# Kernel tuning notes

Hardware: AMD Instinct MI355X
Metric: run time of the kernel (lower is better)

Reference implementation:

```python
import jax, jax.numpy as jnp
import numpy as np

NUM_GRAPHS = 1024
IN_F = 256
HID = 512


def setup_inputs() -> dict:
    key = jax.random.key(0)
    ks = jax.random.split(key, 20)
    s_in = 1.0 / np.sqrt(IN_F)
    s_h = 1.0 / np.sqrt(HID)
    inp = {
        "x": jax.random.normal(ks[0], (200000, IN_F), dtype=jnp.float32),
        "batch": jnp.sort(jax.random.randint(ks[1], (200000,), 0, NUM_GRAPHS)),
        # transforms: Linear(in_features -> hidden)
        "W_mean": jax.random.uniform(ks[2], (IN_F, HID), jnp.float32, -s_in, s_in),
        "b_mean": jax.random.uniform(ks[3], (HID,), jnp.float32, -s_in, s_in),
        "W_max": jax.random.uniform(ks[4], (IN_F, HID), jnp.float32, -s_in, s_in),
        "b_max": jax.random.uniform(ks[5], (HID,), jnp.float32, -s_in, s_in),
        "W_sum": jax.random.uniform(ks[6], (IN_F, HID), jnp.float32, -s_in, s_in),
        "b_sum": jax.random.uniform(ks[7], (HID,), jnp.float32, -s_in, s_in),
        # gates: Linear(hidden -> 1) + sigmoid
        "g_mean_w": jax.random.uniform(ks[8], (HID, 1), jnp.float32, -s_h, s_h),
        "g_mean_b": jax.random.uniform(ks[9], (1,), jnp.float32, -s_h, s_h),
        "g_max_w": jax.random.uniform(ks[10], (HID, 1), jnp.float32, -s_h, s_h),
        "g_max_b": jax.random.uniform(ks[11], (1,), jnp.float32, -s_h, s_h),
        "g_sum_w": jax.random.uniform(ks[12], (HID, 1), jnp.float32, -s_h, s_h),
        "g_sum_b": jax.random.uniform(ks[13], (1,), jnp.float32, -s_h, s_h),
        # output proj: Linear(hidden -> in_features)
        "W_out": jax.random.uniform(ks[14], (HID, IN_F), jnp.float32, -s_h, s_h),
        "b_out": jax.random.uniform(ks[15], (IN_F,), jnp.float32, -s_h, s_h),
        # layer norm params
        "ln_gamma": jnp.ones((IN_F,), jnp.float32),
        "ln_beta": jnp.zeros((IN_F,), jnp.float32),
    }
    return inp


def reference(x, batch, W_mean, b_mean, W_max, b_max, W_sum, b_sum,
              g_mean_w, g_mean_b, g_max_w, g_max_b, g_sum_w, g_sum_b,
              W_out, b_out, ln_gamma, ln_beta):
    # --- segment pools over node dim ---
    sum_pool = jax.ops.segment_sum(x, batch, num_segments=NUM_GRAPHS)  # [G, F]
    counts = jax.ops.segment_sum(jnp.ones((x.shape[0],), x.dtype), batch,
                                 num_segments=NUM_GRAPHS)  # [G]
    mean_pool = sum_pool / jnp.maximum(counts, 1.0)[:, None]
    max_pool = jax.ops.segment_max(x, batch, num_segments=NUM_GRAPHS)
    max_pool = jnp.where(counts[:, None] > 0, max_pool, 0.0)

    # --- per-pool linear transforms ---
    mean_repr = mean_pool @ W_mean + b_mean  # [G, H]
    max_repr = max_pool @ W_max + b_max
    sum_repr = sum_pool @ W_sum + b_sum

    # --- gated fusion ---
    g_mean = jax.nn.sigmoid(mean_repr @ g_mean_w + g_mean_b)  # [G, 1]
    g_max = jax.nn.sigmoid(max_repr @ g_max_w + g_max_b)
    g_sum = jax.nn.sigmoid(sum_repr @ g_sum_w + g_sum_b)
    gates = jax.nn.softmax(jnp.concatenate([g_mean, g_max, g_sum], axis=1), axis=1)
    pooled = (gates[:, 0:1] * mean_repr + gates[:, 1:2] * max_repr
              + gates[:, 2:3] * sum_repr)

    # --- output projection (+dropout as eval identity) + layer norm ---
    emb = pooled @ W_out + b_out  # [G, F]
    mu = jnp.mean(emb, axis=-1, keepdims=True)
    var = jnp.var(emb, axis=-1, keepdims=True)
    emb = (emb - mu) * jax.lax.rsqrt(var + 1e-5) * ln_gamma + ln_beta
    return emb
```

## Files before the change

kernel.cpp:

```cpp
#include <hip/hip_runtime.h>
#include <math.h>

#define NUM_GRAPHS 1024
#define IN_F 256
#define HID 512

typedef __bf16 bf16x4 __attribute__((ext_vector_type(4)));
typedef __bf16 bf16x8 __attribute__((ext_vector_type(8)));
typedef float  f32x4  __attribute__((ext_vector_type(4)));

__global__ __launch_bounds__(256) void prep_kernel(
    const float* __restrict__ Wm, const float* __restrict__ Wx, const float* __restrict__ Wsm,
    __bf16* __restrict__ wt,
    const int* __restrict__ batch, int N, int* __restrict__ seg)
{
    int b = blockIdx.x;
    if (b < 96) {
        __shared__ float tile[64][65];
        int z  = b / 32;
        int kt = (b % 32) / 8, nt = b % 8;
        const float* W = (z==0) ? Wm : (z==1) ? Wx : Wsm;
        __bf16* Wt = wt + (size_t)z * HID * IN_F;
        int k0 = kt * 64, n0 = nt * 64;
        int r  = threadIdx.x >> 2;
        int c0 = (threadIdx.x & 3) * 16;
        #pragma unroll
        for (int j = 0; j < 4; ++j) {
            float4 v = *(const float4*)&W[(size_t)(k0 + r)*HID + n0 + c0 + j*4];
            tile[r][c0+j*4+0] = v.x; tile[r][c0+j*4+1] = v.y;
            tile[r][c0+j*4+2] = v.z; tile[r][c0+j*4+3] = v.w;
        }
        __syncthreads();
        #pragma unroll
        for (int j = 0; j < 4; ++j) {
            bf16x4 o;
            o.x = (__bf16)tile[c0+j*4+0][r];
            o.y = (__bf16)tile[c0+j*4+1][r];
            o.z = (__bf16)tile[c0+j*4+2][r];
            o.w = (__bf16)tile[c0+j*4+3][r];
            *(bf16x4*)&Wt[(size_t)(n0 + r)*IN_F + k0 + c0 + j*4] = o;
        }
    } else {
        int i = (b - 96) * 256 + threadIdx.x;
        if (i <= N) {
            int cur  = (i < N) ? batch[i] : NUM_GRAPHS;
            int prev = (i == 0) ? -1 : batch[i-1];
            for (int g = prev + 1; g <= cur; ++g) seg[g] = i;
        }
    }
}

__global__ __launch_bounds__(256) void pool_kernel(
    const float* __restrict__ x, const int* __restrict__ seg,
    __bf16* __restrict__ pool_mean, __bf16* __restrict__ pool_max,
    __bf16* __restrict__ pool_sum)
{
    int g = blockIdx.x;
    int start = seg[g], end = seg[g+1];
    int cnt = end - start;
    int w = threadIdx.x >> 6, lane = threadIdx.x & 63;
    const float4* x4 = (const float4*)x;
    float4 s = make_float4(0.f, 0.f, 0.f, 0.f);
    float4 m = make_float4(-INFINITY, -INFINITY, -INFINITY, -INFINITY);
    int r = start + w;
    for (; r + 12 < end; r += 16) {
        float4 v0 = x4[(size_t)(r     )*64 + lane];
        float4 v1 = x4[(size_t)(r +  4)*64 + lane];
        float4 v2 = x4[(size_t)(r +  8)*64 + lane];
        float4 v3 = x4[(size_t)(r + 12)*64 + lane];
        s.x += (v0.x+v1.x)+(v2.x+v3.x); s.y += (v0.y+v1.y)+(v2.y+v3.y);
        s.z += (v0.z+v1.z)+(v2.z+v3.z); s.w += (v0.w+v1.w)+(v2.w+v3.w);
        m.x = fmaxf(m.x, fmaxf(fmaxf(v0.x,v1.x), fmaxf(v2.x,v3.x)));
        m.y = fmaxf(m.y, fmaxf(fmaxf(v0.y,v1.y), fmaxf(v2.y,v3.y)));
        m.z = fmaxf(m.z, fmaxf(fmaxf(v0.z,v1.z), fmaxf(v2.z,v3.z)));
        m.w = fmaxf(m.w, fmaxf(fmaxf(v0.w,v1.w), fmaxf(v2.w,v3.w)));
    }
    for (; r < end; r += 4) {
        float4 v = x4[(size_t)r*64 + lane];
        s.x += v.x; s.y += v.y; s.z += v.z; s.w += v.w;
        m.x = fmaxf(m.x, v.x); m.y = fmaxf(m.y, v.y);
        m.z = fmaxf(m.z, v.z); m.w = fmaxf(m.w, v.w);
    }
    __shared__ float4 Ls[4][64];
    __shared__ float4 Lm[4][64];
    Ls[w][lane] = s; Lm[w][lane] = m;
    __syncthreads();
    if (w == 0) {
        float4 s0 = Ls[0][lane], s1 = Ls[1][lane], s2 = Ls[2][lane], s3 = Ls[3][lane];
        float4 m0 = Lm[0][lane], m1 = Lm[1][lane], m2 = Lm[2][lane], m3 = Lm[3][lane];
        float4 st, mt;
        st.x = (s0.x+s1.x)+(s2.x+s3.x); st.y = (s0.y+s1.y)+(s2.y+s3.y);
        st.z = (s0.z+s1.z)+(s2.z+s3.z); st.w = (s0.w+s1.w)+(s2.w+s3.w);
        mt.x = fmaxf(fmaxf(m0.x,m1.x), fmaxf(m2.x,m3.x));
        mt.y = fmaxf(fmaxf(m0.y,m1.y), fmaxf(m2.y,m3.y));
        mt.z = fmaxf(fmaxf(m0.z,m1.z), fmaxf(m2.z,m3.z));
        mt.w = fmaxf(fmaxf(m0.w,m1.w), fmaxf(m2.w,m3.w));
        float inv = 1.0f / fmaxf((float)cnt, 1.0f);
        if (cnt == 0) mt = make_float4(0.f, 0.f, 0.f, 0.f);
        bf16x4 sb, mb, xb;
        sb.x = (__bf16)st.x;       sb.y = (__bf16)st.y;
        sb.z = (__bf16)st.z;       sb.w = (__bf16)st.w;
        mb.x = (__bf16)(st.x*inv); mb.y = (__bf16)(st.y*inv);
        mb.z = (__bf16)(st.z*inv); mb.w = (__bf16)(st.w*inv);
        xb.x = (__bf16)mt.x;       xb.y = (__bf16)mt.y;
        xb.z = (__bf16)mt.z;       xb.w = (__bf16)mt.w;
        size_t o = (size_t)g*64 + lane;
        ((bf16x4*)pool_sum)[o]  = sb;
        ((bf16x4*)pool_mean)[o] = mb;
        ((bf16x4*)pool_max)[o]  = xb;
    }
}

__global__ __launch_bounds__(256) void transform_mfma(
    const __bf16* __restrict__ pm, const __bf16* __restrict__ px, const __bf16* __restrict__ ps,
    const __bf16* __restrict__ wtm, const __bf16* __restrict__ wtx, const __bf16* __restrict__ wts,
    const float* __restrict__ bm_, const float* __restrict__ bx_, const float* __restrict__ bs_,
    float* __restrict__ r_mean, float* __restrict__ r_max, float* __restrict__ r_sum)
{
    int z = blockIdx.z;
    const __bf16* A  = (z==0) ? pm  : (z==1) ? px  : ps;
    const __bf16* Bt = (z==0) ? wtm : (z==1) ? wtx : wts;
    const float* bias= (z==0) ? bm_ : (z==1) ? bx_ : bs_;
    float* R         = (z==0) ? r_mean : (z==1) ? r_max : r_sum;

    int bn0 = blockIdx.x * 64;
    int bm0 = blockIdx.y * 64;
    int w = threadIdx.x >> 6, lane = threadIdx.x & 63;
    int qm = lane >> 4, rm = lane & 15;
    const bf16x8* Arow = (const bf16x8*)(A + (size_t)(bm0 + w*16 + rm)*IN_F);
    const bf16x8* B0 = (const bf16x8*)(Bt + (size_t)(bn0 +  0 + rm)*IN_F);
    const bf16x8* B1 = (const bf16x8*)(Bt + (size_t)(bn0 + 16 + rm)*IN_F);
    const bf16x8* B2 = (const bf16x8*)(Bt + (size_t)(bn0 + 32 + rm)*IN_F);
    const bf16x8* B3 = (const bf16x8*)(Bt + (size_t)(bn0 + 48 + rm)*IN_F);
    f32x4 a0 = {0.f,0.f,0.f,0.f}, a1 = a0, a2 = a0, a3 = a0;
    #pragma unroll
    for (int j = 0; j < 8; ++j) {
        int fi = j*4 + qm;
        bf16x8 af = Arow[fi];
        a0 = __builtin_amdgcn_mfma_f32_16x16x32_bf16(af, B0[fi], a0, 0, 0, 0);
        a1 = __builtin_amdgcn_mfma_f32_16x16x32_bf16(af, B1[fi], a1, 0, 0, 0);
        a2 = __builtin_amdgcn_mfma_f32_16x16x32_bf16(af, B2[fi], a2, 0, 0, 0);
        a3 = __builtin_amdgcn_mfma_f32_16x16x32_bf16(af, B3[fi], a3, 0, 0, 0);
    }
    int row0 = bm0 + w*16 + qm*4;
    float b0 = bias[bn0 +  0 + rm], b1 = bias[bn0 + 16 + rm];
    float b2 = bias[bn0 + 32 + rm], b3 = bias[bn0 + 48 + rm];
    #pragma unroll
    for (int r = 0; r < 4; ++r) {
        float* Rr = R + (size_t)(row0 + r)*HID;
        Rr[bn0 +  0 + rm] = a0[r] + b0;
        Rr[bn0 + 16 + rm] = a1[r] + b1;
        Rr[bn0 + 32 + rm] = a2[r] + b2;
        Rr[bn0 + 48 + rm] = a3[r] + b3;
    }
}

#define EM 4
__global__ __launch_bounds__(256) void gate_outproj_ln(
    const float* __restrict__ r_mean, const float* __restrict__ r_max, const float* __restrict__ r_sum,
    const float* __restrict__ gwm, const float* __restrict__ gbm,
    const float* __restrict__ gwx, const float* __restrict__ gbx,
    const float* __restrict__ gws, const float* __restrict__ gbs,
    const float* __restrict__ Wout, const float* __restrict__ bout,
    const float* __restrict__ gamma, const float* __restrict__ beta,
    float* __restrict__ out)
{
    int g0 = blockIdx.x * EM;
    int tid = threadIdx.x;
    __shared__ float Rm[EM][HID], Rx[EM][HID], Rs[EM][HID];
    __shared__ float Ps[EM][HID];
    __shared__ float Es[EM][IN_F];
    __shared__ float wgt[EM][3];

    const float4* rm4 = (const float4*)(r_mean + (size_t)g0*HID);
    const float4* rx4 = (const float4*)(r_max  + (size_t)g0*HID);
    const float4* rs4 = (const float4*)(r_sum  + (size_t)g0*HID);
    #pragma unroll
    for (int i = 0; i < 2; ++i) {
        int idx = tid + i*256;
        ((float4*)Rm)[idx] = rm4[idx];
        ((float4*)Rx)[idx] = rx4[idx];
        ((float4*)Rs)[idx] = rs4[idx];
    }
    __syncthreads();

    int w = tid >> 6, lane = tid & 63;
    float dm = 0.f, dx = 0.f, dsv = 0.f;
    #pragma unroll
    for (int j = 0; j < 8; ++j) {
        int k = lane + j*64;
        dm  += Rm[w][k] * gwm[k];
        dx  += Rx[w][k] * gwx[k];
        dsv += Rs[w][k] * gws[k];
    }
    #pragma unroll
    for (int off = 32; off > 0; off >>= 1) {
        dm  += __shfl_xor(dm,  off, 64);
        dx  += __shfl_xor(dx,  off, 64);
        dsv += __shfl_xor(dsv, off, 64);
    }
    if (lane == 0) {
        float sm = 1.f/(1.f + expf(-(dm  + gbm[0])));
        float sx = 1.f/(1.f + expf(-(dx  + gbx[0])));
        float ss = 1.f/(1.f + expf(-(dsv + gbs[0])));
        float em = expf(sm), ex = expf(sx), es = expf(ss);
        float inv = 1.f/(em + ex + es);
        wgt[w][0] = em*inv; wgt[w][1] = ex*inv; wgt[w][2] = es*inv;
    }
    __syncthreads();

    #pragma unroll
    for (int i = 0; i < 8; ++i) {
        int e = tid + i*256;
        int j = e >> 9, k = e & 511;
        Ps[j][k] = wgt[j][0]*Rm[j][k] + wgt[j][1]*Rx[j][k] + wgt[j][2]*Rs[j][k];
    }
    __syncthreads();

    float a0 = 0.f, a1 = 0.f, a2 = 0.f, a3 = 0.f;
    int f = tid;
    for (int k = 0; k < HID; k += 4) {
        float4 p0 = *(const float4*)&Ps[0][k];
        float4 p1 = *(const float4*)&Ps[1][k];
        float4 p2 = *(const float4*)&Ps[2][k];
        float4 p3 = *(const float4*)&Ps[3][k];
        float w0 = Wout[(size_t)(k+0)*IN_F + f];
        float w1 = Wout[(size_t)(k+1)*IN_F + f];
        float w2 = Wout[(size_t)(k+2)*IN_F + f];
        float w3 = Wout[(size_t)(k+3)*IN_F + f];
        a0 += p0.x*w0 + p0.y*w1 + p0.z*w2 + p0.w*w3;
        a1 += p1.x*w0 + p1.y*w1 + p1.z*w2 + p1.w*w3;
        a2 += p2.x*w0 + p2.y*w1 + p2.z*w2 + p2.w*w3;
        a3 += p3.x*w0 + p3.y*w1 + p3.z*w2 + p3.w*w3;
    }
    float bo = bout[f];
    Es[0][f] = a0 + bo; Es[1][f] = a1 + bo; Es[2][f] = a2 + bo; Es[3][f] = a3 + bo;
    __syncthreads();

    float v0 = Es[w][lane], v1 = Es[w][lane+64], v2 = Es[w][lane+128], v3 = Es[w][lane+192];
    float s  = (v0+v1) + (v2+v3);
    float sq = (v0*v0 + v1*v1) + (v2*v2 + v3*v3);
    #pragma unroll
    for (int off = 32; off > 0; off >>= 1) {
        s  += __shfl_xor(s,  off, 64);
        sq += __shfl_xor(sq, off, 64);
    }
    float mu  = s * (1.0f/IN_F);
    float var = sq * (1.0f/IN_F) - mu*mu;
    float rs  = rsqrtf(var + 1e-5f);
    float* orow = out + (size_t)(g0 + w)*IN_F;
    orow[lane]     = (v0-mu)*rs*gamma[lane]     + beta[lane];
    orow[lane+64]  = (v1-mu)*rs*gamma[lane+64]  + beta[lane+64];
    orow[lane+128] = (v2-mu)*rs*gamma[lane+128] + beta[lane+128];
    orow[lane+192] = (v3-mu)*rs*gamma[lane+192] + beta[lane+192];
}

extern "C" void kernel_launch(void* const* d_in, const int* in_sizes, int n_in,
                              void* d_out, int out_size, void* d_ws, size_t ws_size,
                              hipStream_t stream)
{
    const float* x        = (const float*)d_in[0];
    const int*   batch    = (const int*)d_in[1];
    const float* W_mean   = (const float*)d_in[2];
    const float* b_mean   = (const float*)d_in[3];
    const float* W_max    = (const float*)d_in[4];
    const float* b_max    = (const float*)d_in[5];
    const float* W_sum    = (const float*)d_in[6];
    const float* b_sum    = (const float*)d_in[7];
    const float* g_mean_w = (const float*)d_in[8];
    const float* g_mean_b = (const float*)d_in[9];
    const float* g_max_w  = (const float*)d_in[10];
    const float* g_max_b  = (const float*)d_in[11];
    const float* g_sum_w  = (const float*)d_in[12];
    const float* g_sum_b  = (const float*)d_in[13];
    const float* W_out    = (const float*)d_in[14];
    const float* b_out    = (const float*)d_in[15];
    const float* ln_gamma = (const float*)d_in[16];
    const float* ln_beta  = (const float*)d_in[17];
    float* out = (float*)d_out;
    int N = in_sizes[1];

    float* ws      = (float*)d_ws;
    float* r_mean  = ws;
    float* r_max   = r_mean + (size_t)NUM_GRAPHS*HID;
    float* r_sum   = r_max  + (size_t)NUM_GRAPHS*HID;
    __bf16* pool_bf = (__bf16*)(r_sum + (size_t)NUM_GRAPHS*HID);
    __bf16* pm  = pool_bf;
    __bf16* px  = pm + (size_t)NUM_GRAPHS*IN_F;
    __bf16* psu = px + (size_t)NUM_GRAPHS*IN_F;
    __bf16* wt  = psu + (size_t)NUM_GRAPHS*IN_F;
    __bf16* wtm = wt;
    __bf16* wtx = wtm + (size_t)HID*IN_F;
    __bf16* wts = wtx + (size_t)HID*IN_F;
    int* seg    = (int*)(wts + (size_t)HID*IN_F);

    int bnd_blocks = (N + 1 + 255) / 256;
    prep_kernel<<<96 + bnd_blocks, 256, 0, stream>>>(W_mean, W_max, W_sum, wt, batch, N, seg);

    pool_kernel<<<NUM_GRAPHS, 256, 0, stream>>>(x, seg, pm, px, psu);

    dim3 gridC(HID/64, NUM_GRAPHS/64, 3);
    transform_mfma<<<gridC, 256, 0, stream>>>(pm, px, psu, wtm, wtx, wts,
                                              b_mean, b_max, b_sum,
                                              r_mean, r_max, r_sum);

    gate_outproj_ln<<<NUM_GRAPHS/EM, 256, 0, stream>>>(r_mean, r_max, r_sum,
                                                       g_mean_w, g_mean_b, g_max_w, g_max_b,
                                                       g_sum_w, g_sum_b,
                                                       W_out, b_out, ln_gamma, ln_beta, out);
}
```

Baseline: 394.3 us.

## Merge prep into pool kernel, use MFMA bf16 output projection and bf16 intermediates

Removes the separate segment-boundary pass: each pool block now finds its start and end with a binary search on the sorted batch, and weight transposition runs in extra blocks of the same launch, which drops one kernel launch. The transform outputs are stored as bf16 instead of fp32 to halve intermediate traffic. The output projection switches from scalar FP32 loops to bf16 MFMA using a pre-transposed W_out, with 16 graphs per block. The cost is lower precision in the gated fusion and projection path.

```diff
diff --git a/kernel.cpp b/kernel.cpp
--- a/kernel.cpp
+++ b/kernel.cpp
@@ -9,24 +9,49 @@
 typedef __bf16 bf16x8 __attribute__((ext_vector_type(8)));
 typedef float  f32x4  __attribute__((ext_vector_type(4)));
 
-__global__ __launch_bounds__(256) void prep_kernel(
+__device__ __forceinline__ int lower_bound_i(const int* __restrict__ b, int n, int v) {
+    int lo = 0, hi = n;
+    while (lo < hi) {
+        int mid = (lo + hi) >> 1;
+        if (b[mid] < v) lo = mid + 1; else hi = mid;
+    }
+    return lo;
+}
+
+__device__ __forceinline__ float bdot8(bf16x8 a, float4 w0, float4 w1) {
+    return (float)a[0]*w0.x + (float)a[1]*w0.y + (float)a[2]*w0.z + (float)a[3]*w0.w
+         + (float)a[4]*w1.x + (float)a[5]*w1.y + (float)a[6]*w1.z + (float)a[7]*w1.w;
+}
+
+__global__ __launch_bounds__(256) void pool_prep_kernel(
+    const float* __restrict__ x, const int* __restrict__ batch, int N,
+    __bf16* __restrict__ pool_mean, __bf16* __restrict__ pool_max,
+    __bf16* __restrict__ pool_sum,
     const float* __restrict__ Wm, const float* __restrict__ Wx, const float* __restrict__ Wsm,
+    const float* __restrict__ Wout,
     __bf16* __restrict__ wt,
-    const int* __restrict__ batch, int N, int* __restrict__ seg)
+    __bf16* __restrict__ wtout)
 {
-    int b = blockIdx.x;
-    if (b < 96) {
+    if (blockIdx.x >= NUM_GRAPHS) {
         __shared__ float tile[64][65];
-        int z  = b / 32;
-        int kt = (b % 32) / 8, nt = b % 8;
-        const float* W = (z==0) ? Wm : (z==1) ? Wx : Wsm;
-        __bf16* Wt = wt + (size_t)z * HID * IN_F;
-        int k0 = kt * 64, n0 = nt * 64;
+        int tb = blockIdx.x - NUM_GRAPHS;
+        int z = tb >> 5, t = tb & 31;
+        const float* S; __bf16* D; int SC, SR, r0, cb;
+        if (z < 3) {
+            S = (z==0) ? Wm : (z==1) ? Wx : Wsm;
+            D = wt + (size_t)z * HID * IN_F;
+            SR = 256; SC = 512;
+            r0 = (t >> 3) * 64; cb = (t & 7) * 64;
+        } else {
+            S = Wout; D = wtout;
+            SR = 512; SC = 256;
+            r0 = (t >> 2) * 64; cb = (t & 3) * 64;
+        }
         int r  = threadIdx.x >> 2;
         int c0 = (threadIdx.x & 3) * 16;
         #pragma unroll
         for (int j = 0; j < 4; ++j) {
-            float4 v = *(const float4*)&W[(size_t)(k0 + r)*HID + n0 + c0 + j*4];
+            float4 v = *(const float4*)&S[(size_t)(r0 + r)*SC + cb + c0 + j*4];
             tile[r][c0+j*4+0] = v.x; tile[r][c0+j*4+1] = v.y;
             tile[r][c0+j*4+2] = v.z; tile[r][c0+j*4+3] = v.w;
         }
@@ -38,25 +63,15 @@
             o.y = (__bf16)tile[c0+j*4+1][r];
             o.z = (__bf16)tile[c0+j*4+2][r];
             o.w = (__bf16)tile[c0+j*4+3][r];
-            *(bf16x4*)&Wt[(size_t)(n0 + r)*IN_F + k0 + c0 + j*4] = o;
-        }
-    } else {
-        int i = (b - 96) * 256 + threadIdx.x;
-        if (i <= N) {
-            int cur  = (i < N) ? batch[i] : NUM_GRAPHS;
-            int prev = (i == 0) ? -1 : batch[i-1];
-            for (int g = prev + 1; g <= cur; ++g) seg[g] = i;
-        }
-    }
-}
-
-__global__ __launch_bounds__(256) void pool_kernel(
-    const float* __restrict__ x, const int* __restrict__ seg,
-    __bf16* __restrict__ pool_mean, __bf16* __restrict__ pool_max,
-    __bf16* __restrict__ pool_sum)
-{
+            *(bf16x4*)&D[(size_t)(cb + r)*SR + r0 + c0 + j*4] = o;
+        }
+        return;
+    }
     int g = blockIdx.x;
-    int start = seg[g], end = seg[g+1];
+    __shared__ int sb[2];
+    if (threadIdx.x < 2) sb[threadIdx.x] = lower_bound_i(batch, N, g + (int)threadIdx.x);
+    __syncthreads();
+    int start = sb[0], end = sb[1];
     int cnt = end - start;
     int w = threadIdx.x >> 6, lane = threadIdx.x & 63;
     const float4* x4 = (const float4*)x;
@@ -97,17 +112,17 @@
         mt.w = fmaxf(fmaxf(m0.w,m1.w), fmaxf(m2.w,m3.w));
         float inv = 1.0f / fmaxf((float)cnt, 1.0f);
         if (cnt == 0) mt = make_float4(0.f, 0.f, 0.f, 0.f);
-        bf16x4 sb, mb, xb;
-        sb.x = (__bf16)st.x;       sb.y = (__bf16)st.y;
-        sb.z = (__bf16)st.z;       sb.w = (__bf16)st.w;
-        mb.x = (__bf16)(st.x*inv); mb.y = (__bf16)(st.y*inv);
-        mb.z = (__bf16)(st.z*inv); mb.w = (__bf16)(st.w*inv);
-        xb.x = (__bf16)mt.x;       xb.y = (__bf16)mt.y;
-        xb.z = (__bf16)mt.z;       xb.w = (__bf16)mt.w;
+        bf16x4 sb4, mb4, xb4;
+        sb4.x = (__bf16)st.x;       sb4.y = (__bf16)st.y;
+        sb4.z = (__bf16)st.z;       sb4.w = (__bf16)st.w;
+        mb4.x = (__bf16)(st.x*inv); mb4.y = (__bf16)(st.y*inv);
+        mb4.z = (__bf16)(st.z*inv); mb4.w = (__bf16)(st.w*inv);
+        xb4.x = (__bf16)mt.x;       xb4.y = (__bf16)mt.y;
+        xb4.z = (__bf16)mt.z;       xb4.w = (__bf16)mt.w;
         size_t o = (size_t)g*64 + lane;
-        ((bf16x4*)pool_sum)[o]  = sb;
-        ((bf16x4*)pool_mean)[o] = mb;
-        ((bf16x4*)pool_max)[o]  = xb;
+        ((bf16x4*)pool_sum)[o]  = sb4;
+        ((bf16x4*)pool_mean)[o] = mb4;
+        ((bf16x4*)pool_max)[o]  = xb4;
     }
 }
 
@@ -115,13 +130,13 @@
     const __bf16* __restrict__ pm, const __bf16* __restrict__ px, const __bf16* __restrict__ ps,
     const __bf16* __restrict__ wtm, const __bf16* __restrict__ wtx, const __bf16* __restrict__ wts,
     const float* __restrict__ bm_, const float* __restrict__ bx_, const float* __restrict__ bs_,
-    float* __restrict__ r_mean, float* __restrict__ r_max, float* __restrict__ r_sum)
+    __bf16* __restrict__ r_mean, __bf16* __restrict__ r_max, __bf16* __restrict__ r_sum)
 {
     int z = blockIdx.z;
     const __bf16* A  = (z==0) ? pm  : (z==1) ? px  : ps;
     const __bf16* Bt = (z==0) ? wtm : (z==1) ? wtx : wts;
     const float* bias= (z==0) ? bm_ : (z==1) ? bx_ : bs_;
-    float* R         = (z==0) ? r_mean : (z==1) ? r_max : r_sum;
+    __bf16* R        = (z==0) ? r_mean : (z==1) ? r_max : r_sum;
 
     int bn0 = blockIdx.x * 64;
     int bm0 = blockIdx.y * 64;
@@ -147,112 +162,141 @@
     float b2 = bias[bn0 + 32 + rm], b3 = bias[bn0 + 48 + rm];
     #pragma unroll
     for (int r = 0; r < 4; ++r) {
-        float* Rr = R + (size_t)(row0 + r)*HID;
-        Rr[bn0 +  0 + rm] = a0[r] + b0;
-        Rr[bn0 + 16 + rm] = a1[r] + b1;
-        Rr[bn0 + 32 + rm] = a2[r] + b2;
-        Rr[bn0 + 48 + rm] = a3[r] + b3;
-    }
-}
-
-#define EM 4
-__global__ __launch_bounds__(256) void gate_outproj_ln(
-    const float* __restrict__ r_mean, const float* __restrict__ r_max, const float* __restrict__ r_sum,
+        __bf16* Rr = R + (size_t)(row0 + r)*HID;
+        Rr[bn0 +  0 + rm] = (__bf16)(a0[r] + b0);
+        Rr[bn0 + 16 + rm] = (__bf16)(a1[r] + b1);
+        Rr[bn0 + 32 + rm] = (__bf16)(a2[r] + b2);
+        Rr[bn0 + 48 + rm] = (__bf16)(a3[r] + b3);
+    }
+}
+
+#define EM 16
+__global__ __launch_bounds__(256) void fused_tail(
+    const __bf16* __restrict__ r_mean, const __bf16* __restrict__ r_max, const __bf16* __restrict__ r_sum,
     const float* __restrict__ gwm, const float* __restrict__ gbm,
     const float* __restrict__ gwx, const float* __restrict__ gbx,
     const float* __restrict__ gws, const float* __restrict__ gbs,
-    const float* __restrict__ Wout, const float* __restrict__ bout,
+    const __bf16* __restrict__ wtout, const float* __restrict__ bout,
     const float* __restrict__ gamma, const float* __restrict__ beta,
     float* __restrict__ out)
 {
     int g0 = blockIdx.x * EM;
     int tid = threadIdx.x;
-    __shared__ float Rm[EM][HID], Rx[EM][HID], Rs[EM][HID];
-    __shared__ float Ps[EM][HID];
-    __shared__ float Es[EM][IN_F];
+    int w = tid >> 6, lane = tid & 63;
+    int qm = lane >> 4, rm = lane & 15;
+
+    __shared__ __align__(16) char smem_raw[3*EM*HID*2];
+    __bf16 (*R3)[EM][HID] = (__bf16(*)[EM][HID])smem_raw;
+    float (*Es)[264] = (float(*)[264])smem_raw;
+    __shared__ __bf16 pooled[EM][520];
     __shared__ float wgt[EM][3];
 
-    const float4* rm4 = (const float4*)(r_mean + (size_t)g0*HID);
-    const float4* rx4 = (const float4*)(r_max  + (size_t)g0*HID);
-    const float4* rs4 = (const float4*)(r_sum  + (size_t)g0*HID);
-    #pragma unroll
-    for (int i = 0; i < 2; ++i) {
-        int idx = tid + i*256;
-        ((float4*)Rm)[idx] = rm4[idx];
-        ((float4*)Rx)[idx] = rx4[idx];
-        ((float4*)Rs)[idx] = rs4[idx];
-    }
-    __syncthreads();
-
-    int w = tid >> 6, lane = tid & 63;
-    float dm = 0.f, dx = 0.f, dsv = 0.f;
-    #pragma unroll
-    for (int j = 0; j < 8; ++j) {
-        int k = lane + j*64;
-        dm  += Rm[w][k] * gwm[k];
-        dx  += Rx[w][k] * gwx[k];
-        dsv += Rs[w][k] * gws[k];
-    }
-    #pragma unroll
-    for (int off = 32; off > 0; off >>= 1) {
-        dm  += __shfl_xor(dm,  off, 64);
-        dx  += __shfl_xor(dx,  off, 64);
-        dsv += __shfl_xor(dsv, off, 64);
-    }
-    if (lane == 0) {
-        float sm = 1.f/(1.f + expf(-(dm  + gbm[0])));
-        float sx = 1.f/(1.f + expf(-(dx  + gbx[0])));
-        float ss = 1.f/(1.f + expf(-(dsv + gbs[0])));
-        float em = expf(sm), ex = expf(sx), es = expf(ss);
-        float inv = 1.f/(em + ex + es);
-        wgt[w][0] = em*inv; wgt[w][1] = ex*inv; wgt[w][2] = es*inv;
-    }
-    __syncthreads();
-
-    #pragma unroll
-    for (int i = 0; i < 8; ++i) {
-        int e = tid + i*256;
-        int j = e >> 9, k = e & 511;
-        Ps[j][k] = wgt[j][0]*Rm[j][k] + wgt[j][1]*Rx[j][k] + wgt[j][2]*Rs[j][k];
-    }
-    __syncthreads();
-
-    float a0 = 0.f, a1 = 0.f, a2 = 0.f, a3 = 0.f;
-    int f = tid;
-    for (int k = 0; k < HID; k += 4) {
-        float4 p0 = *(const float4*)&Ps[0][k];
-        float4 p1 = *(const float4*)&Ps[1][k];
-        float4 p2 = *(const float4*)&Ps[2][k];
-        float4 p3 = *(const float4*)&Ps[3][k];
-        float w0 = Wout[(size_t)(k+0)*IN_F + f];
-        float w1 = Wout[(size_t)(k+1)*IN_F + f];
-        float w2 = Wout[(size_t)(k+2)*IN_F + f];
-        float w3 = Wout[(size_t)(k+3)*IN_F + f];
-        a0 += p0.x*w0 + p0.y*w1 + p0.z*w2 + p0.w*w3;
-        a1 += p1.x*w0 + p1.y*w1 + p1.z*w2 + p1.w*w3;
-        a2 += p2.x*w0 + p2.y*w1 + p2.z*w2 + p2.w*w3;
-        a3 += p3.x*w0 + p3.y*w1 + p3.z*w2 + p3.w*w3;
-    }
-    float bo = bout[f];
-    Es[0][f] = a0 + bo; Es[1][f] = a1 + bo; Es[2][f] = a2 + bo; Es[3][f] = a3 + bo;
-    __syncthreads();
-
-    float v0 = Es[w][lane], v1 = Es[w][lane+64], v2 = Es[w][lane+128], v3 = Es[w][lane+192];
-    float s  = (v0+v1) + (v2+v3);
-    float sq = (v0*v0 + v1*v1) + (v2*v2 + v3*v3);
-    #pragma unroll
-    for (int off = 32; off > 0; off >>= 1) {
-        s  += __shfl_xor(s,  off, 64);
-        sq += __shfl_xor(sq, off, 64);
-    }
-    float mu  = s * (1.0f/IN_F);
-    float var = sq * (1.0f/IN_F) - mu*mu;
-    float rs  = rsqrtf(var + 1e-5f);
-    float* orow = out + (size_t)(g0 + w)*IN_F;
-    orow[lane]     = (v0-mu)*rs*gamma[lane]     + beta[lane];
-    orow[lane+64]  = (v1-mu)*rs*gamma[lane+64]  + beta[lane+64];
-    orow[lane+128] = (v2-mu)*rs*gamma[lane+128] + beta[lane+128];
-    orow[lane+192] = (v3-mu)*rs*gamma[lane+192] + beta[lane+192];
+    #pragma unroll
+    for (int i = 0; i < 12; ++i) {
+        int c = tid + i*256;
+        int z = c >> 10, rem = c & 1023;
+        int g = rem >> 6, kc = (rem & 63) * 8;
+        const __bf16* src = (z==0) ? r_mean : (z==1) ? r_max : r_sum;
+        *(bf16x8*)&R3[z][g][kc] = *(const bf16x8*)&src[(size_t)(g0 + g)*HID + kc];
+    }
+    __syncthreads();
+
+    float4 wm0 = *(const float4*)&gwm[lane*8], wm1 = *(const float4*)&gwm[lane*8+4];
+    float4 wx0 = *(const float4*)&gwx[lane*8], wx1 = *(const float4*)&gwx[lane*8+4];
+    float4 ws0 = *(const float4*)&gws[lane*8], ws1 = *(const float4*)&gws[lane*8+4];
+    #pragma unroll
+    for (int gi = 0; gi < 4; ++gi) {
+        int g = w*4 + gi;
+        bf16x8 am = *(const bf16x8*)&R3[0][g][lane*8];
+        bf16x8 ax = *(const bf16x8*)&R3[1][g][lane*8];
+        bf16x8 as = *(const bf16x8*)&R3[2][g][lane*8];
+        float dm  = bdot8(am, wm0, wm1);
+        float dx  = bdot8(ax, wx0, wx1);
+        float dsv = bdot8(as, ws0, ws1);
+        #pragma unroll
+        for (int off = 32; off > 0; off >>= 1) {
+            dm  += __shfl_xor(dm,  off, 64);
+            dx  += __shfl_xor(dx,  off, 64);
+            dsv += __shfl_xor(dsv, off, 64);
+        }
+        if (lane == 0) {
+            float sm = 1.f/(1.f + expf(-(dm  + gbm[0])));
+            float sx = 1.f/(1.f + expf(-(dx  + gbx[0])));
+            float ss = 1.f/(1.f + expf(-(dsv + gbs[0])));
+            float em = expf(sm), ex = expf(sx), es = expf(ss);
+            float inv = 1.f/(em + ex + es);
+            wgt[g][0] = em*inv; wgt[g][1] = ex*inv; wgt[g][2] = es*inv;
+        }
+    }
+    __syncthreads();
+
+    #pragma unroll
+    for (int i = 0; i < 4; ++i) {
+        int c = tid + i*256;
+        int g = c >> 6, kc = (c & 63) * 8;
+        bf16x8 am = *(const bf16x8*)&R3[0][g][kc];
+        bf16x8 ax = *(const bf16x8*)&R3[1][g][kc];
+        bf16x8 as = *(const bf16x8*)&R3[2][g][kc];
+        float w0 = wgt[g][0], w1 = wgt[g][1], w2 = wgt[g][2];
+        bf16x8 o;
+        #pragma unroll
+        for (int e = 0; e < 8; ++e)
+            o[e] = (__bf16)(w0*(float)am[e] + w1*(float)ax[e] + w2*(float)as[e]);
+        *(bf16x8*)&pooled[g][kc] = o;
+    }
+    __syncthreads();
+
+    f32x4 ac0 = {0.f,0.f,0.f,0.f}, ac1 = ac0, ac2 = ac0, ac3 = ac0;
+    const __bf16* Bt0 = wtout + (size_t)((w*4+0)*16 + rm)*HID;
+    const __bf16* Bt1 = wtout + (size_t)((w*4+1)*16 + rm)*HID;
+    const __bf16* Bt2 = wtout + (size_t)((w*4+2)*16 + rm)*HID;
+    const __bf16* Bt3 = wtout + (size_t)((w*4+3)*16 + rm)*HID;
+    #pragma unroll
+    for (int kk = 0; kk < 16; ++kk) {
+        int ko = kk*32 + qm*8;
+        bf16x8 af = *(const bf16x8*)&pooled[rm][ko];
+        ac0 = __builtin_amdgcn_mfma_f32_16x16x32_bf16(af, *(const bf16x8*)&Bt0[ko], ac0, 0, 0, 0);
+        ac1 = __builtin_amdgcn_mfma_f32_16x16x32_bf16(af, *(const bf16x8*)&Bt1[ko], ac1, 0, 0, 0);
+        ac2 = __builtin_amdgcn_mfma_f32_16x16x32_bf16(af, *(const bf16x8*)&Bt2[ko], ac2, 0, 0, 0);
+        ac3 = __builtin_amdgcn_mfma_f32_16x16x32_bf16(af, *(const bf16x8*)&Bt3[ko], ac3, 0, 0, 0);
+    }
+    __syncthreads();
+
+    float bo0 = bout[(w*4+0)*16 + rm], bo1 = bout[(w*4+1)*16 + rm];
+    float bo2 = bout[(w*4+2)*16 + rm], bo3 = bout[(w*4+3)*16 + rm];
+    #pragma unroll
+    for (int r = 0; r < 4; ++r) {
+        int g = qm*4 + r;
+        Es[g][(w*4+0)*16 + rm] = ac0[r] + bo0;
+        Es[g][(w*4+1)*16 + rm] = ac1[r] + bo1;
+        Es[g][(w*4+2)*16 + rm] = ac2[r] + bo2;
+        Es[g][(w*4+3)*16 + rm] = ac3[r] + bo3;
+    }
+    __syncthreads();
+
+    float4 ga = *(const float4*)&gamma[lane*4];
+    float4 be = *(const float4*)&beta[lane*4];
+    #pragma unroll
+    for (int i = 0; i < 4; ++i) {
+        int g = w*4 + i;
+        float4 v = *(const float4*)&Es[g][lane*4];
+        float s  = (v.x + v.y) + (v.z + v.w);
+        float sq = (v.x*v.x + v.y*v.y) + (v.z*v.z + v.w*v.w);
+        #pragma unroll
+        for (int off = 32; off > 0; off >>= 1) {
+            s  += __shfl_xor(s,  off, 64);
+            sq += __shfl_xor(sq, off, 64);
+        }
+        float mu  = s * (1.0f/IN_F);
+        float var = sq * (1.0f/IN_F) - mu*mu;
+        float rs  = rsqrtf(var + 1e-5f);
+        float4 o;
+        o.x = (v.x - mu)*rs*ga.x + be.x;
+        o.y = (v.y - mu)*rs*ga.y + be.y;
+        o.z = (v.z - mu)*rs*ga.z + be.z;
+        o.w = (v.w - mu)*rs*ga.w + be.w;
+        *(float4*)&out[(size_t)(g0 + g)*IN_F + lane*4] = o;
+    }
 }
 
 extern "C" void kernel_launch(void* const* d_in, const int* in_sizes, int n_in,
@@ -280,32 +324,29 @@
     float* out = (float*)d_out;
     int N = in_sizes[1];
 
-    float* ws      = (float*)d_ws;
-    float* r_mean  = ws;
-    float* r_max   = r_mean + (size_t)NUM_GRAPHS*HID;
-    float* r_sum   = r_max  + (size_t)NUM_GRAPHS*HID;
-    __bf16* pool_bf = (__bf16*)(r_sum + (size_t)NUM_GRAPHS*HID);
-    __bf16* pm  = pool_bf;
-    __bf16* px  = pm + (size_t)NUM_GRAPHS*IN_F;
-    __bf16* psu = px + (size_t)NUM_GRAPHS*IN_F;
-    __bf16* wt  = psu + (size_t)NUM_GRAPHS*IN_F;
-    __bf16* wtm = wt;
-    __bf16* wtx = wtm + (size_t)HID*IN_F;
-    __bf16* wts = wtx + (size_t)HID*IN_F;
-    int* seg    = (int*)(wts + (size_t)HID*IN_F);
-
-    int bnd_blocks = (N + 1 + 255) / 256;
-    prep_kernel<<<96 + bnd_blocks, 256, 0, stream>>>(W_mean, W_max, W_sum, wt, batch, N, seg);
-
-    pool_kernel<<<NUM_GRAPHS, 256, 0, stream>>>(x, seg, pm, px, psu);
+    __bf16* B = (__bf16*)d_ws;
+    __bf16* pm    = B;
+    __bf16* px    = pm  + (size_t)NUM_GRAPHS*IN_F;
+    __bf16* psu   = px  + (size_t)NUM_GRAPHS*IN_F;
+    __bf16* wtm   = psu + (size_t)NUM_GRAPHS*IN_F;
+    __bf16* wtx   = wtm + (size_t)HID*IN_F;
+    __bf16* wts   = wtx + (size_t)HID*IN_F;
+    __bf16* wtout = wts + (size_t)HID*IN_F;
+    __bf16* r_mean = wtout + (size_t)IN_F*HID;
+    __bf16* r_max  = r_mean + (size_t)NUM_GRAPHS*HID;
+    __bf16* r_sum  = r_max  + (size_t)NUM_GRAPHS*HID;
+
+    pool_prep_kernel<<<NUM_GRAPHS + 128, 256, 0, stream>>>(
+        x, batch, N, pm, px, psu,
+        W_mean, W_max, W_sum, W_out, wtm, wtout);
 
     dim3 gridC(HID/64, NUM_GRAPHS/64, 3);
     transform_mfma<<<gridC, 256, 0, stream>>>(pm, px, psu, wtm, wtx, wts,
                                               b_mean, b_max, b_sum,
                                               r_mean, r_max, r_sum);
 
-    gate_outproj_ln<<<NUM_GRAPHS/EM, 256, 0, stream>>>(r_mean, r_max, r_sum,
-                                                       g_mean_w, g_mean_b, g_max_w, g_max_b,
-                                                       g_sum_w, g_sum_b,
-                                                       W_out, b_out, ln_gamma, ln_beta, out);
-}
+    fused_tail<<<NUM_GRAPHS/EM, 256, 0, stream>>>(r_mean, r_max, r_sum,
+                                                  g_mean_w, g_mean_b, g_max_w, g_max_b,
+                                                  g_sum_w, g_sum_b,
+                                                  wtout, b_out, ln_gamma, ln_beta, out);
+}
```

Result: faster. 345.0 us (-12.5%).
